# Performance work log

Measured on AMD Instinct MI355X. Metric: run time of the kernel, lower is better.

## Reference

```python
import jax, jax.numpy as jnp
import numpy as np

PATCH = 96
STRIDE = PATCH // 2  # 48


def setup_inputs() -> dict:
    key = jax.random.key(0)
    kx = jax.random.fold_in(key, 0)
    x = jax.random.uniform(kx, (8, 4, 1056, 1056), dtype=jnp.float32)
    mu_pristine = jnp.zeros((36,), dtype=jnp.float32)
    cov_pristine = jnp.eye(36, dtype=jnp.float32)
    return {"x": x, "mu_pristine": mu_pristine, "cov_pristine": cov_pristine}


def _extract_patches(x):
    # x: [B, C, H, W] -> overlapping patches [B, C, N, P, P], stride = P//2
    B, C, H, W = x.shape
    nH = (H - PATCH) // STRIDE + 1
    nW = (W - PATCH) // STRIDE + 1
    idx_h = np.arange(nH)[:, None] * STRIDE + np.arange(PATCH)[None, :]  # [nH, P]
    idx_w = np.arange(nW)[:, None] * STRIDE + np.arange(PATCH)[None, :]  # [nW, P]
    p = x[:, :, idx_h, :]            # [B, C, nH, P, W]
    p = p[:, :, :, :, idx_w]         # [B, C, nH, P, nW, P]
    p = p.transpose(0, 1, 2, 4, 3, 5)  # [B, C, nH, nW, P, P]
    return p.reshape(B, C, nH * nW, PATCH, PATCH)


def reference(x, mu_pristine, cov_pristine):
    patches = _extract_patches(x)  # [B, C, N, P, P]
    mu = patches.mean(axis=(-2, -1))                    # [B, C, N]
    var = patches.var(axis=(-2, -1), ddof=1)            # unbiased, matches torch.var
    gx = jnp.diff(patches, axis=-1)                     # [B, C, N, P, P-1]
    gy = jnp.diff(patches, axis=-2)                     # [B, C, N, P-1, P]
    grad_mag = jnp.sqrt((gx * gx).mean(axis=(-2, -1)) + (gy * gy).mean(axis=(-2, -1)))
    # torch concatenates [mu, var, grad_mag] along channel dim per patch, then means over patches
    feats = jnp.concatenate([mu, var, grad_mag], axis=1).mean(axis=-1)  # [B, 3C]
    d = feats.shape[1]
    mu0 = mu_pristine[:d]
    cov_inv = jnp.linalg.inv(cov_pristine[:d, :d])
    diff = feats - mu0[None, :]
    dist = jnp.sqrt(((diff @ cov_inv) * diff).sum(axis=1))  # Mahalanobis distance [B]
    return dist.mean()
```

## Files before the change

### kernel.cpp

```cpp
#include <hip/hip_runtime.h>
#include <math.h>

#define PATCH 96
#define STRIDE 48
#define NH 21
#define NW 21
#define NP (NH * NW)
#define BATCH 8
#define CHAN 4
#define NBC (BATCH * CHAN)
#define IMG_H 1056
#define IMG_W 1056
#define NHB 44
#define NCHUNK 22
#define NSTAT 6
#define NPIX 9216.0f
#define NGRAD 9120.0f

__global__ __launch_bounds__(320) void band_stats_kernel(
    const float* __restrict__ x, float* __restrict__ pf) {
  __shared__ float acc[NCHUNK * NSTAT];

  const int t = threadIdx.x;
  const int bc = blockIdx.x / NHB;
  const int hb = blockIdx.x - bc * NHB;
  const bool active = t < 264;
  const int tc = active ? t : 263;
  const int noff = (tc == 263) ? 3 : 4;

  const float* rowbase = x + (size_t)bc * (IMG_H * IMG_W)
                           + (size_t)(hb * 24) * IMG_W
                           + (size_t)(4 * tc);

  float s1 = 0.f, s2 = 0.f, gxi = 0.f, gxb = 0.f, gyi = 0.f, gyb = 0.f;
  const bool bnd_is_gxb = ((tc % 12) == 11);

#define SUMS_GX(A, nxt)                                                  \
  do {                                                                   \
    s1 += (A).x + (A).y + (A).z + (A).w;                                 \
    s2 += (A).x * (A).x + (A).y * (A).y + (A).z * (A).z + (A).w * (A).w; \
    float d1 = (A).y - (A).x, d2 = (A).z - (A).y, d3 = (A).w - (A).z;    \
    float d4 = (nxt) - (A).w;                                            \
    gxi += d1 * d1 + d2 * d2 + d3 * d3;                                  \
    float bd = d4 * d4;                                                  \
    if (bnd_is_gxb) gxb += bd; else gxi += bd;                           \
  } while (0)

  float4 prev;
  {
    const float4 A = *(const float4*)rowbase;
    const float nxt = rowbase[noff];
    SUMS_GX(A, nxt);
    prev = A;
  }
#pragma unroll 4
  for (int r = 1; r < 24; ++r) {
    const float4 A = *(const float4*)(rowbase + (size_t)r * IMG_W);
    const float nxt = rowbase[(size_t)r * IMG_W + noff];
    SUMS_GX(A, nxt);
    const float e0 = A.x - prev.x, e1 = A.y - prev.y,
                e2 = A.z - prev.z, e3 = A.w - prev.w;
    gyi += e0 * e0 + e1 * e1 + e2 * e2 + e3 * e3;
    prev = A;
  }
  if (hb != NHB - 1) {
    const float4 A = *(const float4*)(rowbase + (size_t)24 * IMG_W);
    const float e0 = A.x - prev.x, e1 = A.y - prev.y,
                e2 = A.z - prev.z, e3 = A.w - prev.w;
    gyb = e0 * e0 + e1 * e1 + e2 * e2 + e3 * e3;
  }
#undef SUMS_GX

  for (int i = t; i < NCHUNK * NSTAT; i += 320) acc[i] = 0.f;
  __syncthreads();
  if (active) {
    const int chunk = tc / 12;
    atomicAdd(&acc[chunk * NSTAT + 0], s1);
    atomicAdd(&acc[chunk * NSTAT + 1], s2);
    atomicAdd(&acc[chunk * NSTAT + 2], gxi);
    atomicAdd(&acc[chunk * NSTAT + 3], gxb);
    atomicAdd(&acc[chunk * NSTAT + 4], gyi);
    atomicAdd(&acc[chunk * NSTAT + 5], gyb);
  }
  __syncthreads();
  float* dst = pf + (size_t)(bc * NHB + hb) * (NCHUNK * NSTAT);
  for (int i = t; i < NCHUNK * NSTAT; i += 320) dst[i] = acc[i];
}

__global__ __launch_bounds__(512) void patch_feats_kernel(
    const float* __restrict__ pf, float* __restrict__ featsG) {
  __shared__ float S[NHB * NCHUNK * NSTAT];
  __shared__ float wsum[8][3];

  const int bc = blockIdx.x;
  const int t = threadIdx.x;
  const float* src = pf + (size_t)bc * (NHB * NCHUNK * NSTAT);
  for (int i = t; i < NHB * NCHUNK * NSTAT; i += 512) S[i] = src[i];
  __syncthreads();

  float fmu = 0.f, fvar = 0.f, fg = 0.f;
  if (t < NP) {
    const int ph = t / NW, pw = t - ph * NW;
    const int h0 = 2 * ph;
#define AT(h, c, s) S[((h) * NCHUNK + (c)) * NSTAT + (s)]
    float S1 = 0.f, S2 = 0.f, Gx = 0.f, Gy = 0.f;
#pragma unroll
    for (int hh = 0; hh < 4; ++hh) {
      const int h = h0 + hh;
      S1 += AT(h, pw, 0) + AT(h, pw + 1, 0);
      S2 += AT(h, pw, 1) + AT(h, pw + 1, 1);
      Gx += AT(h, pw, 2) + AT(h, pw, 3) + AT(h, pw + 1, 2);
      Gy += AT(h, pw, 4) + AT(h, pw + 1, 4);
    }
#pragma unroll
    for (int hh = 0; hh < 3; ++hh) {
      const int h = h0 + hh;
      Gy += AT(h, pw, 5) + AT(h, pw + 1, 5);
    }
#undef AT
    fmu = S1 / NPIX;
    fvar = (S2 - S1 * S1 / NPIX) / (NPIX - 1.f);
    fg = sqrtf((Gx + Gy) / NGRAD);
  }
#pragma unroll
  for (int off = 32; off > 0; off >>= 1) {
    fmu += __shfl_xor(fmu, off);
    fvar += __shfl_xor(fvar, off);
    fg += __shfl_xor(fg, off);
  }
  const int wave = t >> 6;
  if ((t & 63) == 0) { wsum[wave][0] = fmu; wsum[wave][1] = fvar; wsum[wave][2] = fg; }
  __syncthreads();
  if (t == 0) {
    float m = 0.f, v = 0.f, g = 0.f;
#pragma unroll
    for (int w = 0; w < 8; ++w) { m += wsum[w][0]; v += wsum[w][1]; g += wsum[w][2]; }
    const int b = bc / CHAN, c = bc - b * CHAN;
    featsG[b * 12 + 0 + c] = m / (float)NP;
    featsG[b * 12 + 4 + c] = v / (float)NP;
    featsG[b * 12 + 8 + c] = g / (float)NP;
  }
}

__global__ __launch_bounds__(64) void finalize_kernel(
    const float* __restrict__ featsG, const float* __restrict__ mu0_full,
    const float* __restrict__ cov_full, float* __restrict__ out) {
  __shared__ float feats_s[96];
  __shared__ double inv_s[12][12];
  __shared__ float dist[BATCH];

  const int t = threadIdx.x;
  feats_s[t] = featsG[t];
  if (t < 32) feats_s[64 + t] = featsG[64 + t];

  double M[12];
#pragma unroll
  for (int r = 0; r < 12; ++r) {
    double v = 0.0;
    if (t < 12) v = (double)cov_full[r * 36 + t];
    else if (t < 24) v = (t - 12 == r) ? 1.0 : 0.0;
    M[r] = v;
  }

#pragma unroll
  for (int k = 0; k < 12; ++k) {
    const double piv = __shfl(M[k], k);
    const double ip = 1.0 / piv;
    M[k] *= ip;
#pragma unroll
    for (int r = 0; r < 12; ++r) {
      if (r == k) continue;
      const double f = __shfl(M[r], k);
      M[r] -= f * M[k];
    }
  }

  if (t >= 12 && t < 24) {
    const int j = t - 12;
#pragma unroll
    for (int r = 0; r < 12; ++r) inv_s[r][j] = M[r];
  }
  __syncthreads();

  if (t < BATCH) {
    double acc = 0.0;
    double d[12];
#pragma unroll
    for (int i = 0; i < 12; ++i)
      d[i] = (double)feats_s[t * 12 + i] - (double)mu0_full[i];
#pragma unroll
    for (int i = 0; i < 12; ++i) {
      double row = 0.0;
#pragma unroll
      for (int j = 0; j < 12; ++j) row += inv_s[i][j] * d[j];
      acc += d[i] * row;
    }
    dist[t] = (float)sqrt(acc);
  }
  __syncthreads();
  if (t == 0) {
    float m = 0.f;
#pragma unroll
    for (int b = 0; b < BATCH; ++b) m += dist[b];
    out[0] = m / (float)BATCH;
  }
}

extern "C" void kernel_launch(void* const* d_in, const int* in_sizes, int n_in,
                              void* d_out, int out_size, void* d_ws, size_t ws_size,
                              hipStream_t stream) {
  const float* x   = (const float*)d_in[0];
  const float* mu0 = (const float*)d_in[1];
  const float* cov = (const float*)d_in[2];
  float* out = (float*)d_out;
  float* pf     = (float*)d_ws;
  float* featsG = pf + (size_t)NBC * NHB * NCHUNK * NSTAT;

  band_stats_kernel<<<NBC * NHB, 320, 0, stream>>>(x, pf);
  patch_feats_kernel<<<NBC, 512, 0, stream>>>(pf, featsG);
  finalize_kernel<<<1, 64, 0, stream>>>(featsG, mu0, cov, out);
}
```

Before: 224.7 us.

## Fuse finalize into patch kernel via last-block ticket and batch row loads

Removes the separate finalize launch: each patch_feats block bumps a global ticket with acquire-release atomics, and the last block to arrive computes the 12x12 inverse and the Mahalanobis mean. The band-stats loop is restructured to issue eight row loads up front per 8-row block, with the trailing boundary row loaded before the loop, to expose memory-level parallelism. It also adds an occupancy hint to launch_bounds. The trade-offs are more register pressure and a global counter that must be reset correctly between calls.

```diff
diff --git a/kernel.cpp b/kernel.cpp
--- a/kernel.cpp
+++ b/kernel.cpp
@@ -17,7 +17,9 @@
 #define NPIX 9216.0f
 #define NGRAD 9120.0f
 
-__global__ __launch_bounds__(320) void band_stats_kernel(
+__device__ unsigned int g_ticket = 0;
+
+__global__ __launch_bounds__(320, 6) void band_stats_kernel(
     const float* __restrict__ x, float* __restrict__ pf) {
   __shared__ float acc[NCHUNK * NSTAT];
 
@@ -34,6 +36,9 @@
 
   float s1 = 0.f, s2 = 0.f, gxi = 0.f, gxb = 0.f, gyi = 0.f, gyb = 0.f;
   const bool bnd_is_gxb = ((tc % 12) == 11);
+
+  const int r24 = (hb == NHB - 1) ? 23 : 24;
+  const float4 B = *(const float4*)(rowbase + (size_t)r24 * IMG_W);
 
 #define SUMS_GX(A, nxt)                                                  \
   do {                                                                   \
@@ -46,30 +51,34 @@
     if (bnd_is_gxb) gxb += bd; else gxi += bd;                           \
   } while (0)
 
+#define GY(P, Q, acc_)                                                   \
+  do {                                                                   \
+    float e0 = (Q).x - (P).x, e1 = (Q).y - (P).y,                        \
+          e2 = (Q).z - (P).z, e3 = (Q).w - (P).w;                        \
+    acc_ += e0 * e0 + e1 * e1 + e2 * e2 + e3 * e3;                       \
+  } while (0)
+
   float4 prev;
-  {
-    const float4 A = *(const float4*)rowbase;
-    const float nxt = rowbase[noff];
-    SUMS_GX(A, nxt);
-    prev = A;
-  }
-#pragma unroll 4
-  for (int r = 1; r < 24; ++r) {
-    const float4 A = *(const float4*)(rowbase + (size_t)r * IMG_W);
-    const float nxt = rowbase[(size_t)r * IMG_W + noff];
-    SUMS_GX(A, nxt);
-    const float e0 = A.x - prev.x, e1 = A.y - prev.y,
-                e2 = A.z - prev.z, e3 = A.w - prev.w;
-    gyi += e0 * e0 + e1 * e1 + e2 * e2 + e3 * e3;
-    prev = A;
-  }
-  if (hb != NHB - 1) {
-    const float4 A = *(const float4*)(rowbase + (size_t)24 * IMG_W);
-    const float e0 = A.x - prev.x, e1 = A.y - prev.y,
-                e2 = A.z - prev.z, e3 = A.w - prev.w;
-    gyb = e0 * e0 + e1 * e1 + e2 * e2 + e3 * e3;
-  }
+#pragma unroll
+  for (int rb = 0; rb < 3; ++rb) {
+    float4 A[8];
+    float nx[8];
+#pragma unroll
+    for (int i = 0; i < 8; ++i) {
+      const float* rp = rowbase + (size_t)(rb * 8 + i) * IMG_W;
+      A[i] = *(const float4*)rp;
+      nx[i] = rp[noff];
+    }
+#pragma unroll
+    for (int i = 0; i < 8; ++i) SUMS_GX(A[i], nx[i]);
+    if (rb > 0) GY(prev, A[0], gyi);
+#pragma unroll
+    for (int i = 0; i < 7; ++i) GY(A[i], A[i + 1], gyi);
+    prev = A[7];
+  }
+  GY(prev, B, gyb);
 #undef SUMS_GX
+#undef GY
 
   for (int i = t; i < NCHUNK * NSTAT; i += 320) acc[i] = 0.f;
   __syncthreads();
@@ -88,9 +97,15 @@
 }
 
 __global__ __launch_bounds__(512) void patch_feats_kernel(
-    const float* __restrict__ pf, float* __restrict__ featsG) {
+    const float* __restrict__ pf, float* __restrict__ featsG,
+    const float* __restrict__ mu0_full, const float* __restrict__ cov_full,
+    float* __restrict__ out) {
   __shared__ float S[NHB * NCHUNK * NSTAT];
   __shared__ float wsum[8][3];
+  __shared__ int is_last_s;
+  __shared__ float feats_s[96];
+  __shared__ double inv_s[12][12];
+  __shared__ float dist[BATCH];
 
   const int bc = blockIdx.x;
   const int t = threadIdx.x;
@@ -136,73 +151,78 @@
 #pragma unroll
     for (int w = 0; w < 8; ++w) { m += wsum[w][0]; v += wsum[w][1]; g += wsum[w][2]; }
     const int b = bc / CHAN, c = bc - b * CHAN;
-    featsG[b * 12 + 0 + c] = m / (float)NP;
-    featsG[b * 12 + 4 + c] = v / (float)NP;
-    featsG[b * 12 + 8 + c] = g / (float)NP;
-  }
-}
-
-__global__ __launch_bounds__(64) void finalize_kernel(
-    const float* __restrict__ featsG, const float* __restrict__ mu0_full,
-    const float* __restrict__ cov_full, float* __restrict__ out) {
-  __shared__ float feats_s[96];
-  __shared__ double inv_s[12][12];
-  __shared__ float dist[BATCH];
-
-  const int t = threadIdx.x;
-  feats_s[t] = featsG[t];
-  if (t < 32) feats_s[64 + t] = featsG[64 + t];
-
-  double M[12];
-#pragma unroll
-  for (int r = 0; r < 12; ++r) {
-    double v = 0.0;
-    if (t < 12) v = (double)cov_full[r * 36 + t];
-    else if (t < 24) v = (t - 12 == r) ? 1.0 : 0.0;
-    M[r] = v;
-  }
-
-#pragma unroll
-  for (int k = 0; k < 12; ++k) {
-    const double piv = __shfl(M[k], k);
-    const double ip = 1.0 / piv;
-    M[k] *= ip;
-#pragma unroll
-    for (int r = 0; r < 12; ++r) {
-      if (r == k) continue;
-      const double f = __shfl(M[r], k);
-      M[r] -= f * M[k];
-    }
-  }
-
-  if (t >= 12 && t < 24) {
-    const int j = t - 12;
-#pragma unroll
-    for (int r = 0; r < 12; ++r) inv_s[r][j] = M[r];
-  }
-  __syncthreads();
-
-  if (t < BATCH) {
-    double acc = 0.0;
-    double d[12];
-#pragma unroll
-    for (int i = 0; i < 12; ++i)
-      d[i] = (double)feats_s[t * 12 + i] - (double)mu0_full[i];
-#pragma unroll
-    for (int i = 0; i < 12; ++i) {
-      double row = 0.0;
-#pragma unroll
-      for (int j = 0; j < 12; ++j) row += inv_s[i][j] * d[j];
-      acc += d[i] * row;
-    }
-    dist[t] = (float)sqrt(acc);
-  }
-  __syncthreads();
-  if (t == 0) {
-    float m = 0.f;
-#pragma unroll
-    for (int b = 0; b < BATCH; ++b) m += dist[b];
-    out[0] = m / (float)BATCH;
+    __hip_atomic_store(&featsG[b * 12 + 0 + c], m / (float)NP,
+                       __ATOMIC_RELEASE, __HIP_MEMORY_SCOPE_AGENT);
+    __hip_atomic_store(&featsG[b * 12 + 4 + c], v / (float)NP,
+                       __ATOMIC_RELEASE, __HIP_MEMORY_SCOPE_AGENT);
+    __hip_atomic_store(&featsG[b * 12 + 8 + c], g / (float)NP,
+                       __ATOMIC_RELEASE, __HIP_MEMORY_SCOPE_AGENT);
+    __threadfence();
+    unsigned old = __hip_atomic_fetch_add(&g_ticket, 1u, __ATOMIC_ACQ_REL,
+                                          __HIP_MEMORY_SCOPE_AGENT);
+    is_last_s = (old == NBC - 1) ? 1 : 0;
+    if (old == NBC - 1)
+      __hip_atomic_store(&g_ticket, 0u, __ATOMIC_RELAXED,
+                         __HIP_MEMORY_SCOPE_AGENT);
+  }
+  __syncthreads();
+
+  if (is_last_s) {
+    if (t < 64) {
+      feats_s[t] = __hip_atomic_load(&featsG[t], __ATOMIC_RELAXED,
+                                     __HIP_MEMORY_SCOPE_AGENT);
+      if (t < 32)
+        feats_s[64 + t] = __hip_atomic_load(&featsG[64 + t], __ATOMIC_RELAXED,
+                                            __HIP_MEMORY_SCOPE_AGENT);
+      double M[12];
+#pragma unroll
+      for (int r = 0; r < 12; ++r) {
+        double v = 0.0;
+        if (t < 12) v = (double)cov_full[r * 36 + t];
+        else if (t < 24) v = (t - 12 == r) ? 1.0 : 0.0;
+        M[r] = v;
+      }
+#pragma unroll
+      for (int k = 0; k < 12; ++k) {
+        const double piv = __shfl(M[k], k);
+        const double ip = 1.0 / piv;
+        M[k] *= ip;
+#pragma unroll
+        for (int r = 0; r < 12; ++r) {
+          if (r == k) continue;
+          const double f = __shfl(M[r], k);
+          M[r] -= f * M[k];
+        }
+      }
+      if (t >= 12 && t < 24) {
+        const int j = t - 12;
+#pragma unroll
+        for (int r = 0; r < 12; ++r) inv_s[r][j] = M[r];
+      }
+    }
+    __syncthreads();
+    if (t < BATCH) {
+      double acc = 0.0;
+      double d[12];
+#pragma unroll
+      for (int i = 0; i < 12; ++i)
+        d[i] = (double)feats_s[t * 12 + i] - (double)mu0_full[i];
+#pragma unroll
+      for (int i = 0; i < 12; ++i) {
+        double row = 0.0;
+#pragma unroll
+        for (int j = 0; j < 12; ++j) row += inv_s[i][j] * d[j];
+        acc += d[i] * row;
+      }
+      dist[t] = (float)sqrt(acc);
+    }
+    __syncthreads();
+    if (t == 0) {
+      float m = 0.f;
+#pragma unroll
+      for (int b = 0; b < BATCH; ++b) m += dist[b];
+      out[0] = m / (float)BATCH;
+    }
   }
 }
 
@@ -217,6 +237,5 @@
   float* featsG = pf + (size_t)NBC * NHB * NCHUNK * NSTAT;
 
   band_stats_kernel<<<NBC * NHB, 320, 0, stream>>>(x, pf);
-  patch_feats_kernel<<<NBC, 512, 0, stream>>>(pf, featsG);
-  finalize_kernel<<<1, 64, 0, stream>>>(featsG, mu0, cov, out);
+  patch_feats_kernel<<<NBC, 512, 0, stream>>>(pf, featsG, mu0, cov, out);
 }
```

Measured after the change: 290.9 us. 29.5% more time.
